# Performance work log

Hardware: AMD Instinct MI355X
Metric: run time of the kernel (lower is better)

The kernel has to match this reference:

```python
import jax, jax.numpy as jnp
import numpy as np


def setup_inputs() -> dict:
    key = jax.random.key(0)
    k1, k2, k3 = jax.random.split(key, 3)
    dim = 192
    x = jax.random.normal(k1, (4, dim, 256, 256), dtype=jnp.float32)
    # Conv2d(5*dim, dim, 1): weight [dim, 5*dim], bias [dim]
    W = jax.random.normal(k2, (dim, 5 * dim), dtype=jnp.float32) * 0.02
    b = jax.random.normal(k3, (dim,), dtype=jnp.float32) * 0.02
    return {"x": x, "W": W, "b": b}


def _shifts(x):
    # Matches torch: cat([x,
    #   pad(x[:,:,:,1:], (0,1)),   # take right neighbor (zero at last col)
    #   pad(x[:,:,:,:-1], (1,0)),  # take left neighbor (zero at first col)
    #   pad(x[:,:,1:,:], (0,0,0,1)),  # take below neighbor (zero at last row)
    #   pad(x[:,:,:-1,:], (0,0,1,0))  # take above neighbor (zero at first row)
    # ], dim=1)
    right = jnp.pad(x[:, :, :, 1:], ((0, 0), (0, 0), (0, 0), (0, 1)))
    left = jnp.pad(x[:, :, :, :-1], ((0, 0), (0, 0), (0, 0), (1, 0)))
    down = jnp.pad(x[:, :, 1:, :], ((0, 0), (0, 0), (0, 1), (0, 0)))
    up = jnp.pad(x[:, :, :-1, :], ((0, 0), (0, 0), (1, 0), (0, 0)))
    return jnp.concatenate([x, right, left, down, up], axis=1)  # [B, 5C, H, W]


def reference(x, W, b):
    xs = _shifts(x)  # [B, 5C, H, W]
    # 1x1 conv == per-pixel matmul over channels
    out = jnp.einsum("bchw,oc->bohw", xs, W) + b[None, :, None, None]
    return out
```

## Files before the change

kernel.cpp:

```cpp
#include <hip/hip_runtime.h>
#include <hip/hip_bf16.h>
#include <stdint.h>

#define CDIM 192
#define KDIM 960
#define HW   65536
#define WI   256

#define OFF_W2    50331648u
#define OFF_BIAS2 50700288u
#define OFF_FLAG2 50701056u
#define NEED2     50701120u
#define OFF_W4    100663296u
#define OFF_BIAS4 101031936u
#define OFF_FLAG4 101032704u
#define NEED4     101032768u

typedef __attribute__((ext_vector_type(8))) short short8;
typedef __attribute__((ext_vector_type(4))) float floatx4;

__device__ __forceinline__ uint16_t f2b(float v) {
    __hip_bfloat16 h = __float2bfloat16(v);
    return *reinterpret_cast<uint16_t*>(&h);
}

__global__ __launch_bounds__(256) void detect_kernel(const uint32_t* __restrict__ xw,
                                                     int* __restrict__ flag) {
    __shared__ int cnt;
    if (threadIdx.x == 0) cnt = 0;
    __syncthreads();
    int local = 0;
    #pragma unroll
    for (int i = 0; i < 4; ++i) {
        int s = threadIdx.x * 4 + i;
        uint32_t d = xw[(size_t)s * 24571];
        uint32_t e = (d >> 7) & 0xFF;
        if (e >= 110 && e <= 130) ++local;
    }
    atomicAdd(&cnt, local);
    __syncthreads();
    if (threadIdx.x == 0) *flag = (cnt >= 512) ? 1 : 0;
}

__global__ __launch_bounds__(256) void prep_kernel(const void* __restrict__ Wsrc,
                                                   const void* __restrict__ bsrc,
                                                   __hip_bfloat16* __restrict__ Wb,
                                                   float* __restrict__ bfp,
                                                   const int* __restrict__ flag) {
    const int f = *flag;
    if (blockIdx.x < 720) {
        int i = blockIdx.x * 256 + threadIdx.x;
        float v = f ? __bfloat162float(((const __hip_bfloat16*)Wsrc)[i])
                    : ((const float*)Wsrc)[i];
        Wb[i] = __float2bfloat16(v);
    } else if (threadIdx.x < CDIM) {
        int j = threadIdx.x;
        bfp[j] = f ? __bfloat162float(((const __hip_bfloat16*)bsrc)[j])
                   : ((const float*)bsrc)[j];
    }
}

__global__ __launch_bounds__(256) void transpose_kernel(const void* __restrict__ xsrc,
                                                        __hip_bfloat16* __restrict__ xt,
                                                        const int* __restrict__ flag,
                                                        int base_b) {
    __shared__ uint16_t lds16[CDIM * 64];
    const int bid = blockIdx.x;
    const int tid = threadIdx.x;
    const int bb = bid >> 10;
    const int b  = base_b + bb;
    const int p0 = (bid & 1023) << 6;
    const int f = *flag;
    if (f) {
        const uint4* xg = (const uint4*)xsrc;
        #pragma unroll
        for (int t = 0; t < 6; ++t) {
            int idx = tid + t * 256;
            int c = idx >> 3, j = idx & 7;
            size_t off = ((size_t)(b * CDIM + c) * HW + p0 + j * 8) >> 3;
            uint4 v = xg[off];
            int col = (j ^ ((c >> 3) & 7)) << 3;
            *(uint4*)&lds16[c * 64 + col] = v;
        }
    } else {
        const float4* xg = (const float4*)xsrc;
        #pragma unroll
        for (int t = 0; t < 6; ++t) {
            int idx = tid + t * 256;
            int c = idx >> 3, j = idx & 7;
            size_t off4 = ((size_t)(b * CDIM + c) * HW + p0 + j * 8) >> 2;
            float4 v0 = xg[off4], v1 = xg[off4 + 1];
            uint32_t w0 = f2b(v0.x) | ((uint32_t)f2b(v0.y) << 16);
            uint32_t w1 = f2b(v0.z) | ((uint32_t)f2b(v0.w) << 16);
            uint32_t w2 = f2b(v1.x) | ((uint32_t)f2b(v1.y) << 16);
            uint32_t w3 = f2b(v1.z) | ((uint32_t)f2b(v1.w) << 16);
            int col = (j ^ ((c >> 3) & 7)) << 3;
            *(uint4*)&lds16[c * 64 + col] = make_uint4(w0, w1, w2, w3);
        }
    }
    __syncthreads();
    uint4* dst = (uint4*)xt + (size_t)(bb * HW + p0) * 24;
    #pragma unroll
    for (int t = 0; t < 6; ++t) {
        int m = tid + t * 256;
        int px = m / 24, c8 = m % 24;
        int colbase = (((px >> 3) ^ (c8 & 7)) << 3) | (px & 7);
        uint32_t d[4];
        #pragma unroll
        for (int wd = 0; wd < 4; ++wd) {
            uint32_t lo = lds16[(c8 * 8 + 2 * wd) * 64 + colbase];
            uint32_t hi = lds16[(c8 * 8 + 2 * wd + 1) * 64 + colbase];
            d[wd] = lo | (hi << 16);
        }
        dst[m] = make_uint4(d[0], d[1], d[2], d[3]);
    }
}

__device__ __forceinline__ void gload16(const void* g, void* l) {
    __builtin_amdgcn_global_load_lds(
        (const __attribute__((address_space(1))) uint32_t*)g,
        (__attribute__((address_space(3))) uint32_t*)l, 16, 0, 0);
}

__global__ __launch_bounds__(256, 2) void gemm_kernel(const __hip_bfloat16* __restrict__ xt,
                                                      const __hip_bfloat16* __restrict__ Wm,
                                                      const float* __restrict__ biasf,
                                                      void* __restrict__ outv,
                                                      const int* __restrict__ flag,
                                                      int base_b) {
    __shared__ char ldsW[2 * 12288];
    const int f = *flag;
    const int tid  = threadIdx.x;
    const int lane = tid & 63, wave = tid >> 6;
    const int quad = lane >> 4, l15 = lane & 15;

    const int nwg  = (int)gridDim.x;
    const int bid0 = (int)blockIdx.x;
    const int wg   = (bid0 & 7) * (nwg >> 3) + (bid0 >> 3);

    const int bb = wg >> 9;
    const int b  = base_b + bb;
    const int r  = wg & 511;
    const int h  = r >> 1;
    const int w0 = (r & 1) << 7;
    const int p0 = h * WI + w0;
    const int obase = (wave >> 1) * 96;
    const int nbase = (wave & 1) * 64;

    const char* gw[3];
    int ldsoff[3];
    #pragma unroll
    for (int t = 0; t < 3; ++t) {
        int chunk = tid + t * 256;
        int kq = chunk / 192, o = chunk % 192;
        gw[t] = (const char*)Wm + ((size_t)o * KDIM + kq * 8) * 2;
        ldsoff[t] = chunk * 16;
    }
    int aoff[6];
    #pragma unroll
    for (int mt = 0; mt < 6; ++mt) {
        int o = obase + mt * 16 + l15;
        aoff[mt] = (quad * 192 + o) * 16;
    }
    const char* xb = (const char*)(xt + (size_t)bb * HW * CDIM);
    int prow[4]; bool w255[4], wzero[4];
    #pragma unroll
    for (int nt = 0; nt < 4; ++nt) {
        int pl = nbase + nt * 16 + l15;
        prow[nt]  = p0 + pl;
        w255[nt]  = ((w0 + pl) == 255);
        wzero[nt] = ((w0 + pl) == 0);
    }

    floatx4 acc[6][4];
    #pragma unroll
    for (int mt = 0; mt < 6; ++mt)
        #pragma unroll
        for (int nt = 0; nt < 4; ++nt)
            acc[mt][nt] = (floatx4){0.f, 0.f, 0.f, 0.f};

    asm volatile("s_waitcnt vmcnt(0) lgkmcnt(0)" ::: "memory");
    __builtin_amdgcn_sched_barrier(0);
    #pragma unroll
    for (int t = 0; t < 3; ++t) gload16(gw[t], ldsW + ldsoff[t]);

    int s = 0, j6 = 0;
    #pragma unroll 2
    for (int step = 0; step < 30; ++step) {
        const int cur = (step & 1) * 12288;
        const int nxt = 12288 - cur;
        const int dp  = (s == 1) ? 1 : (s == 2) ? -1 : (s == 3) ? WI : (s == 4) ? -WI : 0;
        const bool skip = (s == 3 && h == 255) || (s == 4 && h == 0);
        const int dpe = skip ? 0 : dp;

        __builtin_amdgcn_s_barrier();
        __builtin_amdgcn_sched_barrier(0);
        short8 bfr[4]; bool kill[4];
        #pragma unroll
        for (int nt = 0; nt < 4; ++nt) {
            const bool edge = (s == 1 && w255[nt]) || (s == 2 && wzero[nt]);
            kill[nt] = edge || skip;
            const int rowi = edge ? prow[nt] : (prow[nt] + dpe);
            bfr[nt] = *(const short8*)(xb + ((size_t)rowi * CDIM + j6 * 32 + quad * 8) * 2);
        }
        __builtin_amdgcn_sched_barrier(0);
        if (step < 29) {
            #pragma unroll
            for (int t = 0; t < 3; ++t)
                gload16(gw[t] + (size_t)(step + 1) * 64, ldsW + nxt + ldsoff[t]);
        }
        __builtin_amdgcn_sched_barrier(0);
        if (step < 29) asm volatile("s_waitcnt vmcnt(7)" ::: "memory");
        else           asm volatile("s_waitcnt vmcnt(4)" ::: "memory");
        __builtin_amdgcn_sched_barrier(0);
        __builtin_amdgcn_s_barrier();
        __builtin_amdgcn_sched_barrier(0);

        short8 af[6];
        #pragma unroll
        for (int mt = 0; mt < 6; ++mt)
            af[mt] = *(const short8*)(ldsW + cur + aoff[mt]);
        short8 bf[4];
        #pragma unroll
        for (int nt = 0; nt < 4; ++nt)
            bf[nt] = kill[nt] ? (short8){0, 0, 0, 0, 0, 0, 0, 0} : bfr[nt];

        __builtin_amdgcn_s_setprio(1);
        #pragma unroll
        for (int mt = 0; mt < 6; ++mt)
            #pragma unroll
            for (int nt = 0; nt < 4; ++nt)
                acc[mt][nt] = __builtin_amdgcn_mfma_f32_16x16x32_bf16(
                    af[mt], bf[nt], acc[mt][nt], 0, 0, 0);
        __builtin_amdgcn_s_setprio(0);

        if (++j6 == 6) { j6 = 0; ++s; }
    }

    #pragma unroll
    for (int mt = 0; mt < 6; ++mt) {
        int o0 = obase + mt * 16 + quad * 4;
        float bv[4];
        #pragma unroll
        for (int rr = 0; rr < 4; ++rr) bv[rr] = biasf[o0 + rr];
        #pragma unroll
        for (int nt = 0; nt < 4; ++nt) {
            int px = nbase + nt * 16 + l15;
            size_t base = ((size_t)(b * CDIM + o0) * HW) + p0 + px;
            if (f) {
                __hip_bfloat16* out = (__hip_bfloat16*)outv;
                #pragma unroll
                for (int rr = 0; rr < 4; ++rr)
                    out[base + (size_t)rr * HW] = __float2bfloat16(acc[mt][nt][rr] + bv[rr]);
            } else {
                float* out = (float*)outv;
                #pragma unroll
                for (int rr = 0; rr < 4; ++rr)
                    out[base + (size_t)rr * HW] = acc[mt][nt][rr] + bv[rr];
            }
        }
    }
}

__global__ __launch_bounds__(256) void fallback_kernel(const void* __restrict__ xv,
                                                       const void* __restrict__ Wv,
                                                       const void* __restrict__ bv,
                                                       void* __restrict__ outv,
                                                       const int* __restrict__ flag) {
    __shared__ float Wl[KDIM];
    const int f = *flag;
    const int tid = threadIdx.x;
    const int bid = blockIdx.x;
    const int h = bid & 255;
    const int bo = bid >> 8;
    const int o = bo % CDIM;
    const int b = bo / CDIM;
    if (f) {
        const __hip_bfloat16* W16 = (const __hip_bfloat16*)Wv;
        for (int i = tid; i < KDIM; i += 256) Wl[i] = __bfloat162float(W16[(size_t)o * KDIM + i]);
    } else {
        const float* W32 = (const float*)Wv;
        for (int i = tid; i < KDIM; i += 256) Wl[i] = W32[(size_t)o * KDIM + i];
    }
    __syncthreads();
    const size_t pb = (size_t)b * CDIM * HW + (size_t)h * WI + tid;
    float acc = f ? __bfloat162float(((const __hip_bfloat16*)bv)[o]) : ((const float*)bv)[o];
    if (f) {
        const __hip_bfloat16* x = (const __hip_bfloat16*)xv;
        for (int c = 0; c < CDIM; ++c) {
            const __hip_bfloat16* xp = x + pb + (size_t)c * HW;
            float ctr = __bfloat162float(xp[0]);
            float rgt = (tid < 255) ? __bfloat162float(xp[1])   : 0.f;
            float lft = (tid > 0)   ? __bfloat162float(xp[-1])  : 0.f;
            float dwn = (h < 255)   ? __bfloat162float(xp[WI])  : 0.f;
            float up  = (h > 0)     ? __bfloat162float(xp[-WI]) : 0.f;
            acc += ctr * Wl[c] + rgt * Wl[192 + c] + lft * Wl[384 + c]
                 + dwn * Wl[576 + c] + up * Wl[768 + c];
        }
    } else {
        const float* x = (const float*)xv;
        for (int c = 0; c < CDIM; ++c) {
            const float* xp = x + pb + (size_t)c * HW;
            float ctr = xp[0];
            float rgt = (tid < 255) ? xp[1]   : 0.f;
            float lft = (tid > 0)   ? xp[-1]  : 0.f;
            float dwn = (h < 255)   ? xp[WI]  : 0.f;
            float up  = (h > 0)     ? xp[-WI] : 0.f;
            acc += ctr * Wl[c] + rgt * Wl[192 + c] + lft * Wl[384 + c]
                 + dwn * Wl[576 + c] + up * Wl[768 + c];
        }
    }
    size_t oidx = (size_t)bo * HW + (size_t)h * WI + tid;
    if (f) ((__hip_bfloat16*)outv)[oidx] = __float2bfloat16(acc);
    else   ((float*)outv)[oidx] = acc;
}

extern "C" void kernel_launch(void* const* d_in, const int* in_sizes, int n_in,
                              void* d_out, int out_size, void* d_ws, size_t ws_size,
                              hipStream_t stream) {
    const uint32_t* xw = (const uint32_t*)d_in[0];
    char* ws = (char*)d_ws;

    if (ws_size >= NEED4) {
        int* flag = (int*)(ws + OFF_FLAG4);
        __hip_bfloat16* xt = (__hip_bfloat16*)ws;
        __hip_bfloat16* Wb = (__hip_bfloat16*)(ws + OFF_W4);
        float* bfp = (float*)(ws + OFF_BIAS4);
        detect_kernel<<<1, 256, 0, stream>>>(xw, flag);
        prep_kernel<<<721, 256, 0, stream>>>(d_in[1], d_in[2], Wb, bfp, flag);
        transpose_kernel<<<4096, 256, 0, stream>>>(d_in[0], xt, flag, 0);
        gemm_kernel<<<2048, 256, 0, stream>>>(xt, Wb, bfp, d_out, flag, 0);
    } else if (ws_size >= NEED2) {
        int* flag = (int*)(ws + OFF_FLAG2);
        __hip_bfloat16* xt = (__hip_bfloat16*)ws;
        __hip_bfloat16* Wb = (__hip_bfloat16*)(ws + OFF_W2);
        float* bfp = (float*)(ws + OFF_BIAS2);
        detect_kernel<<<1, 256, 0, stream>>>(xw, flag);
        prep_kernel<<<721, 256, 0, stream>>>(d_in[1], d_in[2], Wb, bfp, flag);
        for (int rnd = 0; rnd < 2; ++rnd) {
            transpose_kernel<<<2048, 256, 0, stream>>>(d_in[0], xt, flag, 2 * rnd);
            gemm_kernel<<<1024, 256, 0, stream>>>(xt, Wb, bfp, d_out, flag, 2 * rnd);
        }
    } else {
        int* flag = (int*)ws;
        detect_kernel<<<1, 256, 0, stream>>>(xw, flag);
        fallback_kernel<<<4 * CDIM * 256, 256, 0, stream>>>(d_in[0], d_in[1], d_in[2],
                                                            d_out, flag);
    }
}
```

Before: 571.4 us.

## Prefetch activation fragments two steps ahead with triple-buffered registers

The main K loop is fully unrolled and the per-step global loads of activation (B) fragments now go into a three-slot register ring, issued two iterations ahead of their use. This lets global-load latency for the activations overlap two rounds of MFMA work instead of being waited on in the same step. The vmcnt wait counts are adjusted to match the deeper queue. The cost is more VGPRs for the extra buffered fragments and a larger unrolled code body, which could reduce occupancy.

```diff
diff --git a/kernel.cpp b/kernel.cpp
--- a/kernel.cpp
+++ b/kernel.cpp
@@ -179,39 +179,55 @@
         for (int nt = 0; nt < 4; ++nt)
             acc[mt][nt] = (floatx4){0.f, 0.f, 0.f, 0.f};
 
+    short8 bfr[3][4];
+    bool   kil[3][4];
+
     asm volatile("s_waitcnt vmcnt(0) lgkmcnt(0)" ::: "memory");
     __builtin_amdgcn_sched_barrier(0);
     #pragma unroll
     for (int t = 0; t < 3; ++t) gload16(gw[t], ldsW + ldsoff[t]);
-
-    int s = 0, j6 = 0;
-    #pragma unroll 2
-    for (int step = 0; step < 30; ++step) {
-        const int cur = (step & 1) * 12288;
-        const int nxt = 12288 - cur;
-        const int dp  = (s == 1) ? 1 : (s == 2) ? -1 : (s == 3) ? WI : (s == 4) ? -WI : 0;
-        const bool skip = (s == 3 && h == 255) || (s == 4 && h == 0);
-        const int dpe = skip ? 0 : dp;
-
+    __builtin_amdgcn_sched_barrier(0);
+    #pragma unroll
+    for (int q = 0; q < 2; ++q)
+        #pragma unroll
+        for (int nt = 0; nt < 4; ++nt) {
+            kil[q][nt] = false;
+            bfr[q][nt] = *(const short8*)(xb + ((size_t)prow[nt] * CDIM + q * 32 + quad * 8) * 2);
+        }
+    __builtin_amdgcn_sched_barrier(0);
+
+    #pragma unroll
+    for (int k = 0; k < 30; ++k) {
+        const int cur = (k & 1) * 12288;
         __builtin_amdgcn_s_barrier();
         __builtin_amdgcn_sched_barrier(0);
-        short8 bfr[4]; bool kill[4];
-        #pragma unroll
-        for (int nt = 0; nt < 4; ++nt) {
-            const bool edge = (s == 1 && w255[nt]) || (s == 2 && wzero[nt]);
-            kill[nt] = edge || skip;
-            const int rowi = edge ? prow[nt] : (prow[nt] + dpe);
-            bfr[nt] = *(const short8*)(xb + ((size_t)rowi * CDIM + j6 * 32 + quad * 8) * 2);
-        }
-        __builtin_amdgcn_sched_barrier(0);
-        if (step < 29) {
+        if (k < 29) {
+            const int nxt = 12288 - cur;
             #pragma unroll
             for (int t = 0; t < 3; ++t)
-                gload16(gw[t] + (size_t)(step + 1) * 64, ldsW + nxt + ldsoff[t]);
-        }
-        __builtin_amdgcn_sched_barrier(0);
-        if (step < 29) asm volatile("s_waitcnt vmcnt(7)" ::: "memory");
-        else           asm volatile("s_waitcnt vmcnt(4)" ::: "memory");
+                gload16(gw[t] + (size_t)(k + 1) * 64, ldsW + nxt + ldsoff[t]);
+        }
+        __builtin_amdgcn_sched_barrier(0);
+        if (k + 2 < 30) {
+            const int k2 = k + 2;
+            const int s2 = k2 / 6, j62 = k2 % 6;
+            const int dp  = (s2 == 1) ? 1 : (s2 == 2) ? -1 : (s2 == 3) ? WI : (s2 == 4) ? -WI : 0;
+            const bool skip = (s2 == 3 && h == 255) || (s2 == 4 && h == 0);
+            const int dpe = skip ? 0 : dp;
+            const int slot = k2 % 3;
+            #pragma unroll
+            for (int nt = 0; nt < 4; ++nt) {
+                const bool edge = (s2 == 1 && w255[nt]) || (s2 == 2 && wzero[nt]);
+                kil[slot][nt] = (edge || skip);
+                const int rowi = edge ? prow[nt] : (prow[nt] + dpe);
+                bfr[slot][nt] = *(const short8*)(xb +
+                    ((size_t)rowi * CDIM + j62 * 32 + quad * 8) * 2);
+            }
+        }
+        __builtin_amdgcn_sched_barrier(0);
+        if (k < 28)       asm volatile("s_waitcnt vmcnt(11)" ::: "memory");
+        else if (k == 28) asm volatile("s_waitcnt vmcnt(7)" ::: "memory");
+        else              asm volatile("s_waitcnt vmcnt(0)" ::: "memory");
         __builtin_amdgcn_sched_barrier(0);
         __builtin_amdgcn_s_barrier();
         __builtin_amdgcn_sched_barrier(0);
@@ -220,10 +236,11 @@
         #pragma unroll
         for (int mt = 0; mt < 6; ++mt)
             af[mt] = *(const short8*)(ldsW + cur + aoff[mt]);
+        const int cs = k % 3;
         short8 bf[4];
         #pragma unroll
         for (int nt = 0; nt < 4; ++nt)
-            bf[nt] = kill[nt] ? (short8){0, 0, 0, 0, 0, 0, 0, 0} : bfr[nt];
+            bf[nt] = kil[cs][nt] ? (short8){0, 0, 0, 0, 0, 0, 0, 0} : bfr[cs][nt];
 
         __builtin_amdgcn_s_setprio(1);
         #pragma unroll
@@ -233,8 +250,6 @@
                 acc[mt][nt] = __builtin_amdgcn_mfma_f32_16x16x32_bf16(
                     af[mt], bf[nt], acc[mt][nt], 0, 0, 0);
         __builtin_amdgcn_s_setprio(0);
-
-        if (++j6 == 6) { j6 = 0; ++s; }
     }
 
     #pragma unroll
```

New measurement: 591.2 us. +3.5%, slower.
